# Kernel tuning notes

Measured on AMD Instinct MI355X. Metric: run time of the kernel, lower is better.

## Reference

```python
import jax, jax.numpy as jnp
import numpy as np

B, K, D, H, R, MAXP, IMG = 8, 1024, 256, 8, 4, 1024, 224


def _ln(x, g, b, eps=1e-5):
    m = x.mean(-1, keepdims=True)
    v = ((x - m) ** 2).mean(-1, keepdims=True)
    return (x - m) / jnp.sqrt(v + eps) * g + b


def _rope2d(x, coords, cache, image_size):
    b, k, d = x.shape
    half, quarter = d // 2, d // 4
    maxp = cache.shape[0]
    cn = jnp.clip(coords.astype(jnp.float32) / image_size * (maxp - 1), 0, maxp - 1)
    y_idx = cn[..., 0].astype(jnp.int32)
    x_idx = cn[..., 1].astype(jnp.int32)
    yr = cache[y_idx]  # [B,K,quarter,2]
    xr = cache[x_idx]
    xp = x[..., :half].reshape(b, k, quarter, 2)
    yp = x[..., half:].reshape(b, k, quarter, 2)

    def rot(p, r):
        c, s = r[..., 0], r[..., 1]
        p0, p1 = p[..., 0], p[..., 1]
        return jnp.stack([p0 * c - p1 * s, p0 * s + p1 * c], -1).reshape(b, k, half)

    return jnp.concatenate([rot(xp, xr), rot(yp, yr)], -1)


def _mha_zero(xn, Wqkv, bqkv, Wo, bo, key_allowed, num_heads):
    # torch MultiheadAttention with an all-zero token appended to key/value
    # BEFORE projection -> extra key = b_k, extra value = b_v per head.
    b, l, d = xn.shape
    hd = d // num_heads
    Wq, Wk, Wv = jnp.split(Wqkv, 3, axis=0)
    bq, bk, bv = jnp.split(bqkv, 3)
    q = (xn @ Wq.T + bq).reshape(b, l, num_heads, hd)
    k = jnp.concatenate([xn @ Wk.T + bk, jnp.broadcast_to(bk, (b, 1, d))], 1)
    v = jnp.concatenate([xn @ Wv.T + bv, jnp.broadcast_to(bv, (b, 1, d))], 1)
    k = k.reshape(b, l + 1, num_heads, hd)
    v = v.reshape(b, l + 1, num_heads, hd)
    scores = jnp.einsum('bqhd,bkhd->bhqk', q, k) / jnp.sqrt(jnp.float32(hd))
    mask = jnp.concatenate([key_allowed, jnp.ones((b, 1), bool)], 1)  # zero slot always visible
    scores = jnp.where(mask[:, None, None, :], scores, -jnp.inf)
    attn = jax.nn.softmax(scores, axis=-1)
    out = jnp.einsum('bhqk,bkhd->bqhd', attn, v).reshape(b, l, d)
    return out @ Wo.T + bo


def setup_inputs() -> dict:
    key = jax.random.key(0)
    ks = jax.random.split(key, 20)
    x = jax.random.normal(ks[0], (B, K, D), dtype=jnp.float32)
    coords = jax.random.randint(ks[1], (B, K, 2), 0, IMG, dtype=jnp.int32)
    ctx_id_labels = jax.random.randint(ks[2], (B, K), 0, 2, dtype=jnp.int32)
    half = D // 2
    theta = 1.0 / (10000.0 ** (jnp.arange(0, half, 2, dtype=jnp.float32) / half))
    pos = jnp.arange(MAXP, dtype=jnp.float32)
    freqs = pos[:, None] * theta[None, :]
    rope_cache = jnp.stack([jnp.cos(freqs), jnp.sin(freqs)], -1)  # [MAXP, D/4, 2]
    s = 0.02
    return {
        'x': x, 'coords': coords, 'ctx_id_labels': ctx_id_labels,
        'target_embed': s * jax.random.normal(ks[3], (1, 1, D)),
        'context_embed': s * jax.random.normal(ks[4], (1, 1, D)),
        'register_tokens': s * jax.random.normal(ks[5], (1, R, D)),
        'rope_cache': rope_cache,
        'norm_g': jnp.ones((D,)), 'norm_b': jnp.zeros((D,)),
        'ctx_Wqkv': s * jax.random.normal(ks[6], (3 * D, D)),
        'ctx_bqkv': jnp.zeros((3 * D,)),
        'ctx_Wo': s * jax.random.normal(ks[7], (D, D)),
        'ctx_bo': jnp.zeros((D,)),
        'tgt_Wqkv': s * jax.random.normal(ks[8], (3 * D, D)),
        'tgt_bqkv': jnp.zeros((3 * D,)),
        'tgt_Wo': s * jax.random.normal(ks[9], (D, D)),
        'tgt_bo': jnp.zeros((D,)),
        'mlpn_g': jnp.ones((D,)), 'mlpn_b': jnp.zeros((D,)),
        'mlp_W1': s * jax.random.normal(ks[10], (4 * D, D)),
        'mlp_b1': jnp.zeros((4 * D,)),
        'mlp_W2': s * jax.random.normal(ks[11], (D, 4 * D)),
        'mlp_b2': jnp.zeros((D,)),
    }


def reference(x, coords, ctx_id_labels, target_embed, context_embed, register_tokens,
              rope_cache, norm_g, norm_b, ctx_Wqkv, ctx_bqkv, ctx_Wo, ctx_bo,
              tgt_Wqkv, tgt_bqkv, tgt_Wo, tgt_bo, mlpn_g, mlpn_b,
              mlp_W1, mlp_b1, mlp_W2, mlp_b2):
    b, k, d = x.shape
    is_ctx = ctx_id_labels > 0
    x = x + jnp.where(is_ctx[..., None], context_embed, target_embed)
    x = _rope2d(x, coords, rope_cache, IMG)
    registers = register_tokens + context_embed  # [1,R,D]
    x = jnp.concatenate([jnp.broadcast_to(registers, (b, R, d)), x], 1)
    is_ctx_f = jnp.concatenate([jnp.ones((b, R), bool), is_ctx], 1)
    xn = _ln(x, norm_g, norm_b)
    # ctx queries self-attend to context(+zero); tgt queries cross-attend to context(+zero)
    out_ctx = _mha_zero(xn, ctx_Wqkv, ctx_bqkv, ctx_Wo, ctx_bo, is_ctx_f, H)
    out_tgt = _mha_zero(xn, tgt_Wqkv, tgt_bqkv, tgt_Wo, tgt_bo, is_ctx_f, H)
    attn_out = jnp.where(is_ctx_f[..., None], out_ctx, out_tgt)
    attn_out = attn_out[:, R:]
    x = x[:, R:]
    x = x + attn_out
    h = _ln(x, mlpn_g, mlpn_b)
    h = jax.nn.gelu(h @ mlp_W1.T + mlp_b1, approximate=False) @ mlp_W2.T + mlp_b2
    return x + h
```

## Files before the change

kernel.cpp:

```cpp
#include <hip/hip_runtime.h>
#include <stdint.h>
#include <stddef.h>

typedef unsigned short u16;
typedef __bf16 bf16t;
typedef bf16t bf16x8 __attribute__((ext_vector_type(8)));
typedef u16 u16x8 __attribute__((ext_vector_type(8)));
typedef u16 u16x4 __attribute__((ext_vector_type(4)));
typedef float f32x4 __attribute__((ext_vector_type(4)));

__device__ __forceinline__ float bf2f(u16 u) {
  unsigned int x = ((unsigned int)u) << 16;
  return __builtin_bit_cast(float, x);
}
__device__ __forceinline__ u16 f2bf(float f) {
  unsigned int x = __builtin_bit_cast(unsigned int, f);
  x += 0x7fffu + ((x >> 16) & 1u);
  return (u16)(x >> 16);
}
__device__ __forceinline__ u16x8 ld8(const u16* p) { return *(const u16x8*)p; }

__device__ __forceinline__ f32x4 mfma_bf16(u16x8 a, u16x8 b, f32x4 c) {
  return __builtin_amdgcn_mfma_f32_16x16x32_bf16(
      __builtin_bit_cast(bf16x8, a), __builtin_bit_cast(bf16x8, b), c, 0, 0, 0);
}
__device__ __forceinline__ void g2lds16(const u16* g, u16* l) {
  __builtin_amdgcn_global_load_lds(
      (const __attribute__((address_space(1))) unsigned int*)g,
      (__attribute__((address_space(3))) unsigned int*)l, 16, 0, 0);
}
__device__ __forceinline__ void stc(u16* p, float v) { *p = f2bf(v); }
__device__ __forceinline__ void stc(float* p, float v) { *p = v; }

__device__ __forceinline__ float fast_erf(float x) {
  const float ax = fabsf(x);
  const float t = 1.0f / (1.0f + 0.3275911f * ax);
  const float y = 1.0f - (((((1.061405429f * t - 1.453152027f) * t) + 1.421413741f) * t
                  - 0.284496736f) * t + 0.254829592f) * t * __expf(-ax * ax);
  return copysignf(y, x);
}


__global__ __launch_bounds__(256) void cvt_kernel(
    const float* __restrict__ cW, const float* __restrict__ tW,
    const float* __restrict__ cWo_, const float* __restrict__ tWo_,
    const float* __restrict__ W1_, const float* __restrict__ W2_,
    const float* __restrict__ cb, const float* __restrict__ tb,
    u16* __restrict__ wA, u16* __restrict__ wB, u16* __restrict__ woc,
    u16* __restrict__ wot, u16* __restrict__ w1b, u16* __restrict__ w2b,
    float* __restrict__ bA, float* __restrict__ bB,
    const int* __restrict__ labels, int* __restrict__ slotm,
    int* __restrict__ inv_c, int* __restrict__ inv_t,
    int* __restrict__ qcnt_c, int* __restrict__ qcnt_t,
    u16* __restrict__ xnc, u16* __restrict__ xnt)
{
  const int blk = blockIdx.x;
  const int tid = threadIdx.x;
  if (blk >= 1026) {
    const int b = blk - 1026;
    const int wave = tid >> 6, lane = tid & 63;
    __shared__ int wcnt[4];
    int base_c = 0, base_t = 0;
    for (int p = 0; p < 4; ++p) {
      const int idx = p * 256 + tid;
      const bool ic = labels[b * 1024 + idx] > 0;
      const unsigned long long mk = __ballot(ic);
      const int lower = __popcll(mk & ((1ull << lane) - 1ull));
      if (lane == 0) wcnt[wave] = __popcll(mk);
      __syncthreads();
      int off = 0, tot = 0;
      #pragma unroll
      for (int i = 0; i < 4; ++i) { if (i < wave) off += wcnt[i]; tot += wcnt[i]; }
      if (ic) {
        const int rank = base_c + off + lower;
        slotm[b * 1024 + idx] = rank;
        inv_c[b * 1024 + rank] = idx;
      } else {
        const int rank = base_t + tid - off - lower;
        slotm[b * 1024 + idx] = rank;
        inv_t[b * 1024 + rank] = idx;
      }
      base_c += tot; base_t += 256 - tot;
      __syncthreads();
    }
    if (tid == 0) { qcnt_c[b] = base_c; qcnt_t[b] = base_t; }
    const int nc4 = base_c + 4;
    const int needA = (nc4 + 127) & ~127;
    const int needB = (base_t + 127) & ~127;
    const u16x8 z8 = {0, 0, 0, 0, 0, 0, 0, 0};
    for (int idx = tid; idx < (needA - nc4) * 32; idx += 256)
      *(u16x8*)&xnc[((size_t)b * 1152 + nc4 + (idx >> 5)) * 256 + (idx & 31) * 8] = z8;
    for (int idx = tid; idx < (needB - base_t) * 32; idx += 256)
      *(u16x8*)&xnt[((size_t)b * 1024 + base_t + (idx >> 5)) * 256 + (idx & 31) * 8] = z8;
    return;
  }
  if (blk >= 1024) {
    const int e = tid * 4;
    if (blk == 1024) {
      #pragma unroll
      for (int j = 0; j < 4; ++j) {
        const int k = e + j;
        bA[k] = (k < 768) ? cb[k] : tb[k - 512];
      }
    } else {
      #pragma unroll
      for (int j = 0; j < 4; ++j) {
        const int k = e + j;
        if (k < 256) bA[1024 + k] = tb[512 + k];
        else if (k < 512) bB[k - 256] = tb[k - 256];
      }
    }
    return;
  }
  const float* s; u16* d;
  if (blk < 192)      { const size_t e = (size_t)blk * 1024; s = cW + e; d = wA + e; }
  else if (blk < 384) { const int lb = blk - 192; const size_t e = (size_t)lb * 1024;
                        s = tW + e; d = (lb < 64) ? (wB + e) : (wA + e + 131072); }
  else if (blk < 448) { const size_t e = (size_t)(blk - 384) * 1024; s = cWo_ + e; d = woc + e; }
  else if (blk < 512) { const size_t e = (size_t)(blk - 448) * 1024; s = tWo_ + e; d = wot + e; }
  else if (blk < 768) { const size_t e = (size_t)(blk - 512) * 1024; s = W1_ + e; d = w1b + e; }
  else                { const size_t e = (size_t)(blk - 768) * 1024; s = W2_ + e; d = w2b + e; }
  const int o = tid * 4;
  const f32x4 v = *(const f32x4*)(s + o);
  u16x4 ov;
  #pragma unroll
  for (int j = 0; j < 4; ++j) ov[j] = f2bf(v[j]);
  *(u16x4*)(d + o) = ov;
}

__global__ __launch_bounds__(256) void prep_kernel(
    const float* __restrict__ x, const int* __restrict__ coords,
    const int* __restrict__ labels, const float* __restrict__ tgt_e,
    const float* __restrict__ ctx_e, const float* __restrict__ regs,
    const float* __restrict__ rope, const float* __restrict__ g,
    const float* __restrict__ bt, const int* __restrict__ slotm,
    float* __restrict__ x0, u16* __restrict__ xnc, u16* __restrict__ xnt)
{
  const int wv = threadIdx.x >> 6, lane = threadIdx.x & 63;
  const int t = blockIdx.x * 4 + wv;
  const int d = lane * 4;
  const int b = t / 1028, l = t - b * 1028;
  f32x4 v;
  u16* dst;
  if (l < 4) {
    const f32x4 rg = *(const f32x4*)&regs[l * 256 + d];
    const f32x4 ce = *(const f32x4*)&ctx_e[d];
    #pragma unroll
    for (int j = 0; j < 4; ++j) v[j] = rg[j] + ce[j];
    dst = &xnc[((size_t)b * 1152 + l) * 256];
  } else {
    const int p = l - 4;
    const bool ic = labels[b * 1024 + p] > 0;
    const float* emb = ic ? ctx_e : tgt_e;
    const int cy = coords[(b * 1024 + p) * 2 + 0];
    const int cx = coords[(b * 1024 + p) * 2 + 1];
    const float fy = fminf(fmaxf(((float)cy / 224.0f) * 1023.0f, 0.0f), 1023.0f);
    const float fx = fminf(fmaxf(((float)cx / 224.0f) * 1023.0f, 0.0f), 1023.0f);
    const int yi = (int)fy, xi = (int)fx;
    const bool second = d >= 128;
    const int ci = second ? yi : xi;
    const int pairi = (d & 127) >> 1;
    const f32x4 rr = *(const f32x4*)&rope[ci * 128 + pairi * 2];
    const int i0 = (second ? 128 : 0) + pairi * 2;
    const size_t base = (size_t)(b * 1024 + p) * 256;
    const f32x4 xv = *(const f32x4*)&x[base + i0];
    const f32x4 ev = *(const f32x4*)&emb[i0];
    const float p0 = xv[0] + ev[0], p1 = xv[1] + ev[1];
    const float p2 = xv[2] + ev[2], p3 = xv[3] + ev[3];
    v[0] = p0 * rr[0] - p1 * rr[1];
    v[1] = p0 * rr[1] + p1 * rr[0];
    v[2] = p2 * rr[2] - p3 * rr[3];
    v[3] = p2 * rr[3] + p3 * rr[2];
    const int rank = slotm[b * 1024 + p];
    dst = ic ? &xnc[((size_t)b * 1152 + 4 + rank) * 256]
             : &xnt[((size_t)b * 1024 + rank) * 256];
  }
  *(f32x4*)&x0[(size_t)t * 256 + d] = v;
  float s1 = v[0] + v[1] + v[2] + v[3];
  #pragma unroll
  for (int off = 1; off < 64; off <<= 1) s1 += __shfl_xor(s1, off);
  const float mean = s1 * (1.0f / 256.0f);
  f32x4 dv;
  float s2 = 0.f;
  #pragma unroll
  for (int j = 0; j < 4; ++j) { dv[j] = v[j] - mean; s2 += dv[j] * dv[j]; }
  #pragma unroll
  for (int off = 1; off < 64; off <<= 1) s2 += __shfl_xor(s2, off);
  const float rstd = rsqrtf(s2 * (1.0f / 256.0f) + 1e-5f);
  const f32x4 gv = *(const f32x4*)&g[d];
  const f32x4 bv = *(const f32x4*)&bt[d];
  u16x4 o;
  #pragma unroll
  for (int j = 0; j < 4; ++j) o[j] = f2bf(dv[j] * rstd * gv[j] + bv[j]);
  *(u16x4*)&dst[d] = o;
}

template <int MI, int EPI, typename CT>
__global__ __launch_bounds__(256) void gemm_bt(
    const u16* __restrict__ A, int lda, const u16* __restrict__ W, int K,
    const float* __restrict__ bias, CT* __restrict__ C, int ldc, int M,
    const float* __restrict__ resid)
{
  constexpr int TM = MI * 32;
  const int mbase = blockIdx.y * TM, nbase = blockIdx.x * 128;
  __shared__ u16 As[TM * 32];
  __shared__ u16 Bs[128 * 32];
  const int tid = threadIdx.x, lane = tid & 63, w = tid >> 6;
  const int quad = lane >> 4, r = lane & 15;
  const int wm = w >> 1, wn = w & 1;
  const int rA = lane >> 2, cA = (lane & 3) * 8;

  f32x4 acc[MI][4];
  #pragma unroll
  for (int i = 0; i < MI; ++i)
    #pragma unroll
    for (int j = 0; j < 4; ++j) acc[i][j] = (f32x4){0.f, 0.f, 0.f, 0.f};

  const int nkt = K >> 5;
  for (int kt = 0; kt < nkt; ++kt) {
    const int k0 = kt * 32;
    #pragma unroll
    for (int j = 0; j < MI / 2; ++j) {
      const int rr = w * (MI * 8) + j * 16;
      g2lds16(&A[(size_t)(mbase + rr + rA) * lda + k0 + cA], &As[rr * 32]);
    }
    #pragma unroll
    for (int j = 0; j < 2; ++j) {
      const int rr = w * 32 + j * 16;
      g2lds16(&W[(size_t)(nbase + rr + rA) * K + k0 + cA], &Bs[rr * 32]);
    }
    __syncthreads();
    u16x8 av[MI], bv[4];
    #pragma unroll
    for (int mi = 0; mi < MI; ++mi) av[mi] = ld8(&As[(wm * (MI * 16) + mi * 16 + r) * 32 + quad * 8]);
    #pragma unroll
    for (int ni = 0; ni < 4; ++ni) bv[ni] = ld8(&Bs[(wn * 64 + ni * 16 + r) * 32 + quad * 8]);
    #pragma unroll
    for (int mi = 0; mi < MI; ++mi)
      #pragma unroll
      for (int ni = 0; ni < 4; ++ni)
        acc[mi][ni] = mfma_bf16(av[mi], bv[ni], acc[mi][ni]);
    __syncthreads();
  }

  #pragma unroll
  for (int mi = 0; mi < MI; ++mi) {
    #pragma unroll
    for (int ni = 0; ni < 4; ++ni) {
      const int col = nbase + wn * 64 + ni * 16 + r;
      const float bs = bias[col];
      const int row0 = mbase + wm * (MI * 16) + mi * 16 + quad * 4;
      #pragma unroll
      for (int i = 0; i < 4; ++i) {
        const int rr2 = row0 + i;
        if (rr2 < M) {
          float v = acc[mi][ni][i] + bs;
          if (EPI == 1) v = 0.5f * v * (1.0f + fast_erf(v * 0.70710678118654752f));
          if (EPI == 2) v += resid[(size_t)rr2 * ldc + col];
          stc(&C[(size_t)rr2 * ldc + col], v);
        }
      }
    }
  }
}

__global__ __launch_bounds__(256) void gemm_qkv(
    const u16* __restrict__ xnc, const u16* __restrict__ xnt,
    const u16* __restrict__ wA, const u16* __restrict__ wB,
    const float* __restrict__ bA, const float* __restrict__ bB,
    u16* __restrict__ qc, u16* __restrict__ qt,
    u16* __restrict__ kbuf, u16* __restrict__ vbufT,
    const int* __restrict__ qcnt_c, const int* __restrict__ qcnt_t)
{
  const int y = blockIdx.y;
  const int nbase = blockIdx.x * 128;
  const u16 *Ap, *Wp; const float* bp;
  int mbase, b;
  bool tgt;
  if (y < 72) {
    tgt = false;
    b = y / 9; const int mt = y - b * 9;
    const int need = (qcnt_c[b] + 4 + 127) & ~127;
    if (mt * 128 >= need) return;
    mbase = b * 1152 + mt * 128;
    Ap = xnc; Wp = wA; bp = bA;
  } else {
    if (nbase >= 256) return;
    tgt = true;
    const int yy = y - 72;
    b = yy >> 3; const int mt = yy & 7;
    const int need = (qcnt_t[b] + 127) & ~127;
    if (mt * 128 >= need) return;
    mbase = b * 1024 + mt * 128;
    Ap = xnt; Wp = wB; bp = bB;
  }

  __shared__ u16 As[128 * 32];
  __shared__ u16 Bs[128 * 32];
  const int tid = threadIdx.x, lane = tid & 63, w = tid >> 6;
  const int quad = lane >> 4, r = lane & 15;
  const int wm = w >> 1, wn = w & 1;
  const int rA = lane >> 2, cA = (lane & 3) * 8;

  f32x4 acc[4][4];
  #pragma unroll
  for (int i = 0; i < 4; ++i)
    #pragma unroll
    for (int j = 0; j < 4; ++j) acc[i][j] = (f32x4){0.f, 0.f, 0.f, 0.f};

  for (int kt = 0; kt < 8; ++kt) {
    const int k0 = kt * 32;
    #pragma unroll
    for (int j = 0; j < 2; ++j) {
      const int rr = w * 32 + j * 16;
      g2lds16(&Ap[(size_t)(mbase + rr + rA) * 256 + k0 + cA], &As[rr * 32]);
      g2lds16(&Wp[(size_t)(nbase + rr + rA) * 256 + k0 + cA], &Bs[rr * 32]);
    }
    __syncthreads();
    u16x8 av[4], bv[4];
    #pragma unroll
    for (int mi = 0; mi < 4; ++mi) av[mi] = ld8(&As[(wm * 64 + mi * 16 + r) * 32 + quad * 8]);
    #pragma unroll
    for (int ni = 0; ni < 4; ++ni) bv[ni] = ld8(&Bs[(wn * 64 + ni * 16 + r) * 32 + quad * 8]);
    #pragma unroll
    for (int mi = 0; mi < 4; ++mi)
      #pragma unroll
      for (int ni = 0; ni < 4; ++ni)
        acc[mi][ni] = mfma_bf16(av[mi], bv[ni], acc[mi][ni]);
    __syncthreads();
  }

  #pragma unroll
  for (int mi = 0; mi < 4; ++mi) {
    #pragma unroll
    for (int ni = 0; ni < 4; ++ni) {
      const int col = nbase + wn * 64 + ni * 16 + r;
      const float bs = bp[col];
      const int row0 = mbase + wm * 64 + mi * 16 + quad * 4;
      if (tgt) {
        #pragma unroll
        for (int i = 0; i < 4; ++i)
          qt[(size_t)(row0 + i) * 256 + col] = f2bf(acc[mi][ni][i] + bs);
      } else if (col < 256) {
        #pragma unroll
        for (int i = 0; i < 4; ++i)
          qc[(size_t)(row0 + i) * 256 + col] = f2bf(acc[mi][ni][i] + bs);
      } else {
        const int slot0 = row0 - b * 1152;
        const int u = col - 256;
        const int z = u >> 9, kv = (u >> 8) & 1, h = (u >> 5) & 7, d = u & 31;
        const size_t zbh = (size_t)(z * 8 + b) * 8 + h;
        if (kv == 0) {
          u16* kp = kbuf + zbh * 36864 + (size_t)slot0 * 32 + d;
          #pragma unroll
          for (int i = 0; i < 4; ++i) kp[i * 32] = f2bf(acc[mi][ni][i] + bs);
        } else {
          u16x4 o;
          #pragma unroll
          for (int i = 0; i < 4; ++i) o[i] = f2bf(acc[mi][ni][i] + bs);
          *(u16x4*)(vbufT + (zbh * 32 + d) * 1152 + slot0) = o;
        }
      }
    }
  }
}

__global__ __launch_bounds__(256) void gemm_wo_fused(
    const u16* __restrict__ Ac, const u16* __restrict__ At,
    const u16* __restrict__ Wc, const u16* __restrict__ Wt,
    const float* __restrict__ bc, const float* __restrict__ btg,
    const int* __restrict__ cnt_c, const int* __restrict__ cnt_t,
    const int* __restrict__ inv_c, const int* __restrict__ inv_t,
    const float* __restrict__ x0, const float* __restrict__ g,
    const float* __restrict__ bt, float* __restrict__ x1,
    u16* __restrict__ hln)
{
  const int z = blockIdx.z;
  const int y = blockIdx.y, b = y >> 4, mt = y & 15;
  const int qn = (z ? cnt_t : cnt_c)[b];
  if (mt * 64 >= ((qn + 63) & ~63)) return;
  const int mbase = b * 1024 + mt * 64;
  const u16* A = z ? At : Ac;
  const u16* W = z ? Wt : Wc;
  const float* bias = z ? btg : bc;
  const int* inv = z ? inv_t : inv_c;

  __shared__ u16 As[64 * 32];
  __shared__ u16 Bs[256 * 32];
  __shared__ float sums[2][64];
  __shared__ float sqs[2][64];
  const int tid = threadIdx.x, lane = tid & 63, w = tid >> 6;
  const int quad = lane >> 4, r = lane & 15;
  const int wm = w >> 1, wn = w & 1;
  const int rA = lane >> 2, cA = (lane & 3) * 8;

  f32x4 acc[2][8];
  #pragma unroll
  for (int i = 0; i < 2; ++i)
    #pragma unroll
    for (int j = 0; j < 8; ++j) acc[i][j] = (f32x4){0.f, 0.f, 0.f, 0.f};

  for (int kt = 0; kt < 8; ++kt) {
    const int k0 = kt * 32;
    g2lds16(&A[(size_t)(mbase + w * 16 + rA) * 256 + k0 + cA], &As[w * 512]);
    #pragma unroll
    for (int j = 0; j < 4; ++j) {
      const int rr = w * 64 + j * 16;
      g2lds16(&W[(size_t)(rr + rA) * 256 + k0 + cA], &Bs[rr * 32]);
    }
    __syncthreads();
    u16x8 av[2], bv[8];
    #pragma unroll
    for (int mi = 0; mi < 2; ++mi) av[mi] = ld8(&As[(wm * 32 + mi * 16 + r) * 32 + quad * 8]);
    #pragma unroll
    for (int ni = 0; ni < 8; ++ni) bv[ni] = ld8(&Bs[(wn * 128 + ni * 16 + r) * 32 + quad * 8]);
    #pragma unroll
    for (int mi = 0; mi < 2; ++mi)
      #pragma unroll
      for (int ni = 0; ni < 8; ++ni)
        acc[mi][ni] = mfma_bf16(av[mi], bv[ni], acc[mi][ni]);
    __syncthreads();
  }

  float biasv[8];
  #pragma unroll
  for (int ni = 0; ni < 8; ++ni) biasv[ni] = bias[wn * 128 + ni * 16 + r];

  #pragma unroll
  for (int mi = 0; mi < 2; ++mi) {
    #pragma unroll
    for (int i = 0; i < 4; ++i) {
      const int lrow = wm * 32 + mi * 16 + quad * 4 + i;
      const int slot = mt * 64 + lrow;
      const int tok = (slot < qn) ? inv[b * 1024 + slot] : 0;
      const float* x0r = &x0[((size_t)b * 1028 + 4 + tok) * 256];
      float s = 0.f, sq = 0.f;
      #pragma unroll
      for (int ni = 0; ni < 8; ++ni) {
        const float v = acc[mi][ni][i] + biasv[ni] + x0r[wn * 128 + ni * 16 + r];
        acc[mi][ni][i] = v;
        s += v; sq += v * v;
      }
      #pragma unroll
      for (int off = 1; off < 16; off <<= 1) {
        s += __shfl_xor(s, off);
        sq += __shfl_xor(sq, off);
      }
      if (r == 0) { sums[wn][lrow] = s; sqs[wn][lrow] = sq; }
    }
  }
  __syncthreads();
  #pragma unroll
  for (int mi = 0; mi < 2; ++mi) {
    #pragma unroll
    for (int i = 0; i < 4; ++i) {
      const int lrow = wm * 32 + mi * 16 + quad * 4 + i;
      const int slot = mt * 64 + lrow;
      if (slot >= qn) continue;
      const float mean = (sums[0][lrow] + sums[1][lrow]) * (1.0f / 256.0f);
      const float var = (sqs[0][lrow] + sqs[1][lrow]) * (1.0f / 256.0f) - mean * mean;
      const float rstd = rsqrtf(var + 1e-5f);
      const int tok = inv[b * 1024 + slot];
      const size_t orow = (size_t)b * 1024 + tok;
      #pragma unroll
      for (int ni = 0; ni < 8; ++ni) {
        const int col = wn * 128 + ni * 16 + r;
        const float v = acc[mi][ni][i];
        x1[orow * 256 + col] = v;
        hln[orow * 256 + col] = f2bf((v - mean) * rstd * g[col] + bt[col]);
      }
    }
  }
}

__global__ __launch_bounds__(256) void attn4_kernel(
    const u16* __restrict__ qc, const u16* __restrict__ qt,
    const u16* __restrict__ kbuf, const u16* __restrict__ vbufT,
    const float* __restrict__ cbq, const float* __restrict__ tbq,
    const int* __restrict__ qcnt_c, const int* __restrict__ qcnt_t,
    u16* __restrict__ o_c, u16* __restrict__ o_t)
{
  const int qbx = blockIdx.x, h = blockIdx.y, b = blockIdx.z;
  const int nc = qcnt_c[b], nt = qcnt_t[b];
  const int cblk = (nc + 63) >> 6, tblk = (nt + 63) >> 6;
  int z, qsb, qn;
  if (qbx < cblk)            { z = 0; qsb = qbx << 6; qn = nc; }
  else if (qbx - cblk < tblk){ z = 1; qsb = (qbx - cblk) << 6; qn = nt; }
  else return;
  const int nc4 = nc + 4;
  const int ntile = (nc4 + 63) >> 6;
  const float* bq = z ? tbq : cbq;
  const u16* Q = z ? qt : qc;
  u16* obuf = z ? o_t : o_c;
  const int qrow0 = z ? (b * 1024 + qsb) : (b * 1152 + 4 + qsb);

  const int tid = threadIdx.x, lane = tid & 63, w = tid >> 6;
  const int quad = lane >> 4, r = lane & 15;
  const float scale = 0.17677669529663687f;

  __shared__ u16 Ks[2][2048];
  __shared__ u16 Vt[2][32 * 66];
  __shared__ u16 Ps[4][16 * 72];

  const u16x8 qf = ld8(&Q[(size_t)(qrow0 + w * 16 + r) * 256 + h * 32 + quad * 8]);

  float s0 = 0.f;
  #pragma unroll
  for (int j = 0; j < 8; ++j) s0 += bf2f(qf[j]) * bq[256 + h * 32 + quad * 8 + j];
  s0 *= scale;
  s0 += __shfl_xor(s0, 16);
  s0 += __shfl_xor(s0, 32);
  float m_ = s0, l_ = 1.0f;
  f32x4 accA, accB;
  #pragma unroll
  for (int i = 0; i < 4; ++i) {
    accA[i] = bq[512 + h * 32 + quad * 4 + i];
    accB[i] = bq[512 + h * 32 + 16 + quad * 4 + i];
  }

  const size_t zbh = (size_t)(z * 8 + b) * 8 + h;
  const u16* kz = kbuf + zbh * 36864;
  const u16* vz = vbufT + zbh * 36864;
  const int dloc = (w << 3) + (lane >> 3), part = lane & 7;

  g2lds16(&kz[w * 512 + lane * 8], &Ks[0][w * 512]);
  u16x8 vv = ld8(&vz[(size_t)dloc * 1152 + part * 8]);

  for (int t = 0; t < ntile; ++t) {
    const int cur = t & 1, nxt = cur ^ 1;
    #pragma unroll
    for (int j = 0; j < 8; ++j) Vt[cur][dloc * 66 + part * 8 + j] = vv[j];
    __syncthreads();
    if (t + 1 < ntile) {
      g2lds16(&kz[(t + 1) * 2048 + w * 512 + lane * 8], &Ks[nxt][w * 512]);
      vv = ld8(&vz[(size_t)dloc * 1152 + (t + 1) * 64 + part * 8]);
    }

    f32x4 sT[4];
    #pragma unroll
    for (int tt = 0; tt < 4; ++tt) {
      const u16x8 kf = ld8(&Ks[cur][(tt * 16 + r) * 32 + quad * 8]);
      sT[tt] = mfma_bf16(kf, qf, (f32x4){0.f, 0.f, 0.f, 0.f});
    }
    const int kb0 = t * 64 + quad * 4;
    float rm = -3.0e38f;
    float sc[4][4];
    #pragma unroll
    for (int tt = 0; tt < 4; ++tt)
      #pragma unroll
      for (int i = 0; i < 4; ++i) {
        const float kbias = (kb0 + tt * 16 + i < nc4) ? 0.0f : -1e30f;
        sc[tt][i] = sT[tt][i] * scale + kbias;
        rm = fmaxf(rm, sc[tt][i]);
      }
    rm = fmaxf(rm, __shfl_xor(rm, 16));
    rm = fmaxf(rm, __shfl_xor(rm, 32));
    const float mn = fmaxf(m_, rm);
    const float al = __expf(m_ - mn);
    m_ = mn;
    float rs = 0.f;
    u16* ps = &Ps[w][r * 72];
    #pragma unroll
    for (int tt = 0; tt < 4; ++tt) {
      u16x4 pk;
      #pragma unroll
      for (int i = 0; i < 4; ++i) {
        const float pv = __expf(sc[tt][i] - mn);
        rs += pv;
        pk[i] = f2bf(pv);
      }
      *(u16x4*)&ps[tt * 16 + quad * 4] = pk;
    }
    rs += __shfl_xor(rs, 16);
    rs += __shfl_xor(rs, 32);
    l_ = l_ * al + rs;
    #pragma unroll
    for (int i = 0; i < 4; ++i) { accA[i] *= al; accB[i] *= al; }
    #pragma unroll
    for (int kk = 0; kk < 2; ++kk) {
      const u16x8 pf = ld8(&Ps[w][r * 72 + kk * 32 + quad * 8]);
      const u16x8 vf0 = ld8(&Vt[cur][r * 66 + kk * 32 + quad * 8]);
      const u16x8 vf1 = ld8(&Vt[cur][(16 + r) * 66 + kk * 32 + quad * 8]);
      accA = mfma_bf16(vf0, pf, accA);
      accB = mfma_bf16(vf1, pf, accB);
    }
  }

  const int qlocal = qsb + w * 16 + r;
  if (qlocal < qn) {
    const float inv = 1.0f / l_;
    u16x4 oa, ob;
    #pragma unroll
    for (int i = 0; i < 4; ++i) { oa[i] = f2bf(accA[i] * inv); ob[i] = f2bf(accB[i] * inv); }
    const size_t orow = (size_t)b * 1024 + qlocal;
    *(u16x4*)&obuf[orow * 256 + h * 32 + quad * 4] = oa;
    *(u16x4*)&obuf[orow * 256 + h * 32 + 16 + quad * 4] = ob;
  }
}

extern "C" void kernel_launch(void* const* d_in, const int* in_sizes, int n_in,
                              void* d_out, int out_size, void* d_ws, size_t ws_size,
                              hipStream_t stream) {
  const float* x      = (const float*)d_in[0];
  const int*   coords = (const int*)d_in[1];
  const int*   labels = (const int*)d_in[2];
  const float* tgt_e  = (const float*)d_in[3];
  const float* ctx_e  = (const float*)d_in[4];
  const float* regs   = (const float*)d_in[5];
  const float* rope   = (const float*)d_in[6];
  const float* ng     = (const float*)d_in[7];
  const float* nb     = (const float*)d_in[8];
  const float* cWqkv  = (const float*)d_in[9];
  const float* cbqkv  = (const float*)d_in[10];
  const float* cWo    = (const float*)d_in[11];
  const float* cbo    = (const float*)d_in[12];
  const float* tWqkv  = (const float*)d_in[13];
  const float* tbqkv  = (const float*)d_in[14];
  const float* tWo    = (const float*)d_in[15];
  const float* tbo    = (const float*)d_in[16];
  const float* mg     = (const float*)d_in[17];
  const float* mbeta  = (const float*)d_in[18];
  const float* W1     = (const float*)d_in[19];
  const float* b1     = (const float*)d_in[20];
  const float* W2     = (const float*)d_in[21];
  const float* b2     = (const float*)d_in[22];

  char* ws = (char*)d_ws;
  float* x0     = (float*)(ws + 0);
  u16*   qc     = (u16*)  (ws + 8421376);
  u16*   xnc    = (u16*)  (ws + 13139968);
  u16*   xnt    = (u16*)  (ws + 17858560);
  u16*   qt     = (u16*)  (ws + 22052864);
  u16*   kbuf   = (u16*)  (ws + 26247168);
  u16*   vbufT  = (u16*)  (ws + 35684352);
  u16*   o_c    = (u16*)  (ws + 45121536);
  u16*   o_t    = (u16*)  (ws + 49315840);
  u16*   wA     = (u16*)  (ws + 53510144);
  u16*   wB     = (u16*)  (ws + 54165504);
  u16*   woc    = (u16*)  (ws + 54296576);
  u16*   wot    = (u16*)  (ws + 54427648);
  u16*   w1b    = (u16*)  (ws + 54558720);
  u16*   w2b    = (u16*)  (ws + 55083008);
  float* bA     = (float*)(ws + 55607296);
  float* bB     = (float*)(ws + 55612416);
  int*   slotm  = (int*)  (ws + 55613440);
  int*   inv_c  = (int*)  (ws + 55646208);
  int*   inv_t  = (int*)  (ws + 55678976);
  int*   qcnt_c = (int*)  (ws + 55711744);
  int*   qcnt_t = (int*)  (ws + 55711776);
  u16*   hln    = (u16*)  (ws + 17858560);
  float* x1     = (float*)(ws + 26247168);
  u16*   hmid   = (u16*)  (ws + 35684352);

  cvt_kernel<<<dim3(1034), 256, 0, stream>>>(cWqkv, tWqkv, cWo, tWo, W1, W2,
                                             cbqkv, tbqkv,
                                             wA, wB, woc, wot, w1b, w2b, bA, bB,
                                             labels, slotm, inv_c, inv_t,
                                             qcnt_c, qcnt_t, xnc, xnt);
  prep_kernel<<<dim3(2056), 256, 0, stream>>>(x, coords, labels, tgt_e, ctx_e,
                                              regs, rope, ng, nb, slotm, x0, xnc, xnt);
  gemm_qkv<<<dim3(10, 136), 256, 0, stream>>>(xnc, xnt, wA, wB, bA, bB,
                                              qc, qt, kbuf, vbufT, qcnt_c, qcnt_t);
  attn4_kernel<<<dim3(17, 8, 8), 256, 0, stream>>>(qc, qt, kbuf, vbufT, cbqkv, tbqkv,
                                                   qcnt_c, qcnt_t, o_c, o_t);
  gemm_wo_fused<<<dim3(1, 128, 2), 256, 0, stream>>>(o_c, o_t, woc, wot, cbo, tbo,
                                                     qcnt_c, qcnt_t, inv_c, inv_t,
                                                     x0, mg, mbeta, x1, hln);
  gemm_bt<4, 1, u16><<<dim3(8, 64), 256, 0, stream>>>(hln, 256, w1b, 256, b1, hmid, 1024, 8192, nullptr);
  gemm_bt<2, 2, float><<<dim3(2, 128), 256, 0, stream>>>(hmid, 1024, w2b, 1024, b2, (float*)d_out, 256, 8192, x1);
}
```

Baseline: 228.4 us.

## Process two query strips per attention block, shrink Wo tiles, move weight casts into prep

The attention kernel now handles two 64-query strips per block, so each K/V tile loaded into LDS is reused by both strips and the grid shrinks from 17 to 9 blocks in x. The Wo+LayerNorm GEMM drops from 64-row to 32-row tiles, doubling its block count to spread work across more CUs. The weight bf16 conversion moves from the compaction kernel into extra blocks of the prep kernel, leaving a small 10-block compaction kernel. Costs include higher register pressure in attention, less tail parallelism there, and more redundant weight loads per row in the Wo GEMM.

New measurement: 220.8 us. 3.3% less time.

```diff
diff --git a/kernel.cpp b/kernel.cpp
--- a/kernel.cpp
+++ b/kernel.cpp
@@ -41,62 +41,19 @@
 }
 
 
-__global__ __launch_bounds__(256) void cvt_kernel(
-    const float* __restrict__ cW, const float* __restrict__ tW,
-    const float* __restrict__ cWo_, const float* __restrict__ tWo_,
-    const float* __restrict__ W1_, const float* __restrict__ W2_,
-    const float* __restrict__ cb, const float* __restrict__ tb,
-    u16* __restrict__ wA, u16* __restrict__ wB, u16* __restrict__ woc,
-    u16* __restrict__ wot, u16* __restrict__ w1b, u16* __restrict__ w2b,
-    float* __restrict__ bA, float* __restrict__ bB,
+__global__ __launch_bounds__(256) void compact_kernel(
     const int* __restrict__ labels, int* __restrict__ slotm,
     int* __restrict__ inv_c, int* __restrict__ inv_t,
     int* __restrict__ qcnt_c, int* __restrict__ qcnt_t,
-    u16* __restrict__ xnc, u16* __restrict__ xnt)
+    u16* __restrict__ xnc, u16* __restrict__ xnt,
+    const float* __restrict__ cb, const float* __restrict__ tb,
+    float* __restrict__ bA, float* __restrict__ bB)
 {
   const int blk = blockIdx.x;
   const int tid = threadIdx.x;
-  if (blk >= 1026) {
-    const int b = blk - 1026;
-    const int wave = tid >> 6, lane = tid & 63;
-    __shared__ int wcnt[4];
-    int base_c = 0, base_t = 0;
-    for (int p = 0; p < 4; ++p) {
-      const int idx = p * 256 + tid;
-      const bool ic = labels[b * 1024 + idx] > 0;
-      const unsigned long long mk = __ballot(ic);
-      const int lower = __popcll(mk & ((1ull << lane) - 1ull));
-      if (lane == 0) wcnt[wave] = __popcll(mk);
-      __syncthreads();
-      int off = 0, tot = 0;
-      #pragma unroll
-      for (int i = 0; i < 4; ++i) { if (i < wave) off += wcnt[i]; tot += wcnt[i]; }
-      if (ic) {
-        const int rank = base_c + off + lower;
-        slotm[b * 1024 + idx] = rank;
-        inv_c[b * 1024 + rank] = idx;
-      } else {
-        const int rank = base_t + tid - off - lower;
-        slotm[b * 1024 + idx] = rank;
-        inv_t[b * 1024 + rank] = idx;
-      }
-      base_c += tot; base_t += 256 - tot;
-      __syncthreads();
-    }
-    if (tid == 0) { qcnt_c[b] = base_c; qcnt_t[b] = base_t; }
-    const int nc4 = base_c + 4;
-    const int needA = (nc4 + 127) & ~127;
-    const int needB = (base_t + 127) & ~127;
-    const u16x8 z8 = {0, 0, 0, 0, 0, 0, 0, 0};
-    for (int idx = tid; idx < (needA - nc4) * 32; idx += 256)
-      *(u16x8*)&xnc[((size_t)b * 1152 + nc4 + (idx >> 5)) * 256 + (idx & 31) * 8] = z8;
-    for (int idx = tid; idx < (needB - base_t) * 32; idx += 256)
-      *(u16x8*)&xnt[((size_t)b * 1024 + base_t + (idx >> 5)) * 256 + (idx & 31) * 8] = z8;
-    return;
-  }
-  if (blk >= 1024) {
+  if (blk >= 8) {
     const int e = tid * 4;
-    if (blk == 1024) {
+    if (blk == 8) {
       #pragma unroll
       for (int j = 0; j < 4; ++j) {
         const int k = e + j;
@@ -112,20 +69,41 @@
     }
     return;
   }
-  const float* s; u16* d;
-  if (blk < 192)      { const size_t e = (size_t)blk * 1024; s = cW + e; d = wA + e; }
-  else if (blk < 384) { const int lb = blk - 192; const size_t e = (size_t)lb * 1024;
-                        s = tW + e; d = (lb < 64) ? (wB + e) : (wA + e + 131072); }
-  else if (blk < 448) { const size_t e = (size_t)(blk - 384) * 1024; s = cWo_ + e; d = woc + e; }
-  else if (blk < 512) { const size_t e = (size_t)(blk - 448) * 1024; s = tWo_ + e; d = wot + e; }
-  else if (blk < 768) { const size_t e = (size_t)(blk - 512) * 1024; s = W1_ + e; d = w1b + e; }
-  else                { const size_t e = (size_t)(blk - 768) * 1024; s = W2_ + e; d = w2b + e; }
-  const int o = tid * 4;
-  const f32x4 v = *(const f32x4*)(s + o);
-  u16x4 ov;
-  #pragma unroll
-  for (int j = 0; j < 4; ++j) ov[j] = f2bf(v[j]);
-  *(u16x4*)(d + o) = ov;
+  const int b = blk;
+  const int wave = tid >> 6, lane = tid & 63;
+  __shared__ int wcnt[4];
+  int base_c = 0, base_t = 0;
+  for (int p = 0; p < 4; ++p) {
+    const int idx = p * 256 + tid;
+    const bool ic = labels[b * 1024 + idx] > 0;
+    const unsigned long long mk = __ballot(ic);
+    const int lower = __popcll(mk & ((1ull << lane) - 1ull));
+    if (lane == 0) wcnt[wave] = __popcll(mk);
+    __syncthreads();
+    int off = 0, tot = 0;
+    #pragma unroll
+    for (int i = 0; i < 4; ++i) { if (i < wave) off += wcnt[i]; tot += wcnt[i]; }
+    if (ic) {
+      const int rank = base_c + off + lower;
+      slotm[b * 1024 + idx] = rank;
+      inv_c[b * 1024 + rank] = idx;
+    } else {
+      const int rank = base_t + tid - off - lower;
+      slotm[b * 1024 + idx] = rank;
+      inv_t[b * 1024 + rank] = idx;
+    }
+    base_c += tot; base_t += 256 - tot;
+    __syncthreads();
+  }
+  if (tid == 0) { qcnt_c[b] = base_c; qcnt_t[b] = base_t; }
+  const int nc4 = base_c + 4;
+  const int needA = (nc4 + 127) & ~127;
+  const int needB = (base_t + 127) & ~127;
+  const u16x8 z8 = {0, 0, 0, 0, 0, 0, 0, 0};
+  for (int idx = tid; idx < (needA - nc4) * 32; idx += 256)
+    *(u16x8*)&xnc[((size_t)b * 1152 + nc4 + (idx >> 5)) * 256 + (idx & 31) * 8] = z8;
+  for (int idx = tid; idx < (needB - base_t) * 32; idx += 256)
+    *(u16x8*)&xnt[((size_t)b * 1024 + base_t + (idx >> 5)) * 256 + (idx & 31) * 8] = z8;
 }
 
 __global__ __launch_bounds__(256) void prep_kernel(
@@ -134,8 +112,31 @@
     const float* __restrict__ ctx_e, const float* __restrict__ regs,
     const float* __restrict__ rope, const float* __restrict__ g,
     const float* __restrict__ bt, const int* __restrict__ slotm,
-    float* __restrict__ x0, u16* __restrict__ xnc, u16* __restrict__ xnt)
+    float* __restrict__ x0, u16* __restrict__ xnc, u16* __restrict__ xnt,
+    const float* __restrict__ cW, const float* __restrict__ tW,
+    const float* __restrict__ cWo_, const float* __restrict__ tWo_,
+    const float* __restrict__ W1_, const float* __restrict__ W2_,
+    u16* __restrict__ wA, u16* __restrict__ wB, u16* __restrict__ woc,
+    u16* __restrict__ wot, u16* __restrict__ w1b, u16* __restrict__ w2b)
 {
+  if (blockIdx.x >= 2056) {
+    const int blk = blockIdx.x - 2056;
+    const float* s; u16* d;
+    if (blk < 192)      { const size_t e = (size_t)blk * 1024; s = cW + e; d = wA + e; }
+    else if (blk < 384) { const int lb = blk - 192; const size_t e = (size_t)lb * 1024;
+                          s = tW + e; d = (lb < 64) ? (wB + e) : (wA + e + 131072); }
+    else if (blk < 448) { const size_t e = (size_t)(blk - 384) * 1024; s = cWo_ + e; d = woc + e; }
+    else if (blk < 512) { const size_t e = (size_t)(blk - 448) * 1024; s = tWo_ + e; d = wot + e; }
+    else if (blk < 768) { const size_t e = (size_t)(blk - 512) * 1024; s = W1_ + e; d = w1b + e; }
+    else                { const size_t e = (size_t)(blk - 768) * 1024; s = W2_ + e; d = w2b + e; }
+    const int o = threadIdx.x * 4;
+    const f32x4 v = *(const f32x4*)(s + o);
+    u16x4 ov;
+    #pragma unroll
+    for (int j = 0; j < 4; ++j) ov[j] = f2bf(v[j]);
+    *(u16x4*)(d + o) = ov;
+    return;
+  }
   const int wv = threadIdx.x >> 6, lane = threadIdx.x & 63;
   const int t = blockIdx.x * 4 + wv;
   const int d = lane * 4;
@@ -376,49 +377,43 @@
     u16* __restrict__ hln)
 {
   const int z = blockIdx.z;
-  const int y = blockIdx.y, b = y >> 4, mt = y & 15;
+  const int y = blockIdx.y, b = y >> 5, mt = y & 31;
   const int qn = (z ? cnt_t : cnt_c)[b];
-  if (mt * 64 >= ((qn + 63) & ~63)) return;
-  const int mbase = b * 1024 + mt * 64;
+  if (mt * 32 >= ((qn + 31) & ~31)) return;
+  const int mbase = b * 1024 + mt * 32;
   const u16* A = z ? At : Ac;
   const u16* W = z ? Wt : Wc;
   const float* bias = z ? btg : bc;
   const int* inv = z ? inv_t : inv_c;
 
-  __shared__ u16 As[64 * 32];
+  __shared__ u16 As[32 * 32];
   __shared__ u16 Bs[256 * 32];
-  __shared__ float sums[2][64];
-  __shared__ float sqs[2][64];
+  __shared__ float sums[2][32];
+  __shared__ float sqs[2][32];
   const int tid = threadIdx.x, lane = tid & 63, w = tid >> 6;
   const int quad = lane >> 4, r = lane & 15;
   const int wm = w >> 1, wn = w & 1;
   const int rA = lane >> 2, cA = (lane & 3) * 8;
 
-  f32x4 acc[2][8];
-  #pragma unroll
-  for (int i = 0; i < 2; ++i)
-    #pragma unroll
-    for (int j = 0; j < 8; ++j) acc[i][j] = (f32x4){0.f, 0.f, 0.f, 0.f};
+  f32x4 acc[8];
+  #pragma unroll
+  for (int j = 0; j < 8; ++j) acc[j] = (f32x4){0.f, 0.f, 0.f, 0.f};
 
   for (int kt = 0; kt < 8; ++kt) {
     const int k0 = kt * 32;
-    g2lds16(&A[(size_t)(mbase + w * 16 + rA) * 256 + k0 + cA], &As[w * 512]);
+    if (w < 2) g2lds16(&A[(size_t)(mbase + w * 16 + rA) * 256 + k0 + cA], &As[w * 512]);
     #pragma unroll
     for (int j = 0; j < 4; ++j) {
       const int rr = w * 64 + j * 16;
       g2lds16(&W[(size_t)(rr + rA) * 256 + k0 + cA], &Bs[rr * 32]);
     }
     __syncthreads();
-    u16x8 av[2], bv[8];
-    #pragma unroll
-    for (int mi = 0; mi < 2; ++mi) av[mi] = ld8(&As[(wm * 32 + mi * 16 + r) * 32 + quad * 8]);
+    const u16x8 av = ld8(&As[(wm * 16 + r) * 32 + quad * 8]);
+    u16x8 bv[8];
     #pragma unroll
     for (int ni = 0; ni < 8; ++ni) bv[ni] = ld8(&Bs[(wn * 128 + ni * 16 + r) * 32 + quad * 8]);
     #pragma unroll
-    for (int mi = 0; mi < 2; ++mi)
-      #pragma unroll
-      for (int ni = 0; ni < 8; ++ni)
-        acc[mi][ni] = mfma_bf16(av[mi], bv[ni], acc[mi][ni]);
+    for (int ni = 0; ni < 8; ++ni) acc[ni] = mfma_bf16(av, bv[ni], acc[ni]);
     __syncthreads();
   }
 
@@ -427,72 +422,70 @@
   for (int ni = 0; ni < 8; ++ni) biasv[ni] = bias[wn * 128 + ni * 16 + r];
 
   #pragma unroll
-  for (int mi = 0; mi < 2; ++mi) {
-    #pragma unroll
-    for (int i = 0; i < 4; ++i) {
-      const int lrow = wm * 32 + mi * 16 + quad * 4 + i;
-      const int slot = mt * 64 + lrow;
-      const int tok = (slot < qn) ? inv[b * 1024 + slot] : 0;
-      const float* x0r = &x0[((size_t)b * 1028 + 4 + tok) * 256];
-      float s = 0.f, sq = 0.f;
-      #pragma unroll
-      for (int ni = 0; ni < 8; ++ni) {
-        const float v = acc[mi][ni][i] + biasv[ni] + x0r[wn * 128 + ni * 16 + r];
-        acc[mi][ni][i] = v;
-        s += v; sq += v * v;
-      }
-      #pragma unroll
-      for (int off = 1; off < 16; off <<= 1) {
-        s += __shfl_xor(s, off);
-        sq += __shfl_xor(sq, off);
-      }
-      if (r == 0) { sums[wn][lrow] = s; sqs[wn][lrow] = sq; }
-    }
+  for (int i = 0; i < 4; ++i) {
+    const int lrow = wm * 16 + quad * 4 + i;
+    const int slot = mt * 32 + lrow;
+    const int tok = (slot < qn) ? inv[b * 1024 + slot] : 0;
+    const float* x0r = &x0[((size_t)b * 1028 + 4 + tok) * 256];
+    float s = 0.f, sq = 0.f;
+    #pragma unroll
+    for (int ni = 0; ni < 8; ++ni) {
+      const float v = acc[ni][i] + biasv[ni] + x0r[wn * 128 + ni * 16 + r];
+      acc[ni][i] = v;
+      s += v; sq += v * v;
+    }
+    #pragma unroll
+    for (int off = 1; off < 16; off <<= 1) {
+      s += __shfl_xor(s, off);
+      sq += __shfl_xor(sq, off);
+    }
+    if (r == 0) { sums[wn][lrow] = s; sqs[wn][lrow] = sq; }
   }
   __syncthreads();
   #pragma unroll
-  for (int mi = 0; mi < 2; ++mi) {
-    #pragma unroll
-    for (int i = 0; i < 4; ++i) {
-      const int lrow = wm * 32 + mi * 16 + quad * 4 + i;
-      const int slot = mt * 64 + lrow;
-      if (slot >= qn) continue;
-      const float mean = (sums[0][lrow] + sums[1][lrow]) * (1.0f / 256.0f);
-      const float var = (sqs[0][lrow] + sqs[1][lrow]) * (1.0f / 256.0f) - mean * mean;
-      const float rstd = rsqrtf(var + 1e-5f);
-      const int tok = inv[b * 1024 + slot];
-      const size_t orow = (size_t)b * 1024 + tok;
-      #pragma unroll
-      for (int ni = 0; ni < 8; ++ni) {
-        const int col = wn * 128 + ni * 16 + r;
-        const float v = acc[mi][ni][i];
-        x1[orow * 256 + col] = v;
-        hln[orow * 256 + col] = f2bf((v - mean) * rstd * g[col] + bt[col]);
-      }
-    }
-  }
-}
-
-__global__ __launch_bounds__(256) void attn4_kernel(
+  for (int i = 0; i < 4; ++i) {
+    const int lrow = wm * 16 + quad * 4 + i;
+    const int slot = mt * 32 + lrow;
+    if (slot >= qn) continue;
+    const float mean = (sums[0][lrow] + sums[1][lrow]) * (1.0f / 256.0f);
+    const float var = (sqs[0][lrow] + sqs[1][lrow]) * (1.0f / 256.0f) - mean * mean;
+    const float rstd = rsqrtf(var + 1e-5f);
+    const int tok = inv[b * 1024 + slot];
+    const size_t orow = (size_t)b * 1024 + tok;
+    #pragma unroll
+    for (int ni = 0; ni < 8; ++ni) {
+      const int col = wn * 128 + ni * 16 + r;
+      const float v = acc[ni][i];
+      x1[orow * 256 + col] = v;
+      hln[orow * 256 + col] = f2bf((v - mean) * rstd * g[col] + bt[col]);
+    }
+  }
+}
+
+__global__ __launch_bounds__(256) void attn5_kernel(
     const u16* __restrict__ qc, const u16* __restrict__ qt,
     const u16* __restrict__ kbuf, const u16* __restrict__ vbufT,
     const float* __restrict__ cbq, const float* __restrict__ tbq,
     const int* __restrict__ qcnt_c, const int* __restrict__ qcnt_t,
     u16* __restrict__ o_c, u16* __restrict__ o_t)
 {
-  const int qbx = blockIdx.x, h = blockIdx.y, b = blockIdx.z;
+  const int px = blockIdx.x, h = blockIdx.y, b = blockIdx.z;
   const int nc = qcnt_c[b], nt = qcnt_t[b];
   const int cblk = (nc + 63) >> 6, tblk = (nt + 63) >> 6;
-  int z, qsb, qn;
-  if (qbx < cblk)            { z = 0; qsb = qbx << 6; qn = nc; }
-  else if (qbx - cblk < tblk){ z = 1; qsb = (qbx - cblk) << 6; qn = nt; }
+  const int cpair = (cblk + 1) >> 1, tpair = (tblk + 1) >> 1;
+  int z, sblk, qn, nblk;
+  if (px < cpair)            { z = 0; sblk = px * 2; qn = nc; nblk = cblk; }
+  else if (px - cpair < tpair){ z = 1; sblk = (px - cpair) * 2; qn = nt; nblk = tblk; }
   else return;
+  const int nstrip = (nblk - sblk >= 2) ? 2 : 1;
   const int nc4 = nc + 4;
   const int ntile = (nc4 + 63) >> 6;
   const float* bq = z ? tbq : cbq;
   const u16* Q = z ? qt : qc;
   u16* obuf = z ? o_t : o_c;
-  const int qrow0 = z ? (b * 1024 + qsb) : (b * 1152 + 4 + qsb);
+  const int qrowbase = z ? (b * 1024) : (b * 1152 + 4);
+  const int qsb0 = sblk * 64;
+  const int qsb1 = (nstrip > 1) ? qsb0 + 64 : qsb0;
 
   const int tid = threadIdx.x, lane = tid & 63, w = tid >> 6;
   const int quad = lane >> 4, r = lane & 15;
@@ -502,20 +495,27 @@
   __shared__ u16 Vt[2][32 * 66];
   __shared__ u16 Ps[4][16 * 72];
 
-  const u16x8 qf = ld8(&Q[(size_t)(qrow0 + w * 16 + r) * 256 + h * 32 + quad * 8]);
-
-  float s0 = 0.f;
-  #pragma unroll
-  for (int j = 0; j < 8; ++j) s0 += bf2f(qf[j]) * bq[256 + h * 32 + quad * 8 + j];
-  s0 *= scale;
-  s0 += __shfl_xor(s0, 16);
-  s0 += __shfl_xor(s0, 32);
-  float m_ = s0, l_ = 1.0f;
-  f32x4 accA, accB;
+  const u16x8 qf0 = ld8(&Q[(size_t)(qrowbase + qsb0 + w * 16 + r) * 256 + h * 32 + quad * 8]);
+  const u16x8 qf1 = ld8(&Q[(size_t)(qrowbase + qsb1 + w * 16 + r) * 256 + h * 32 + quad * 8]);
+
+  float s0a = 0.f, s0b = 0.f;
+  #pragma unroll
+  for (int j = 0; j < 8; ++j) {
+    const float bk = bq[256 + h * 32 + quad * 8 + j];
+    s0a += bf2f(qf0[j]) * bk;
+    s0b += bf2f(qf1[j]) * bk;
+  }
+  s0a *= scale; s0b *= scale;
+  s0a += __shfl_xor(s0a, 16); s0a += __shfl_xor(s0a, 32);
+  s0b += __shfl_xor(s0b, 16); s0b += __shfl_xor(s0b, 32);
+  float m0 = s0a, l0 = 1.0f, m1 = s0b, l1 = 1.0f;
+  f32x4 accA0, accB0, accA1, accB1;
   #pragma unroll
   for (int i = 0; i < 4; ++i) {
-    accA[i] = bq[512 + h * 32 + quad * 4 + i];
-    accB[i] = bq[512 + h * 32 + 16 + quad * 4 + i];
+    accA0[i] = bq[512 + h * 32 + quad * 4 + i];
+    accB0[i] = bq[512 + h * 32 + 16 + quad * 4 + i];
+    accA1[i] = accA0[i];
+    accB1[i] = accB0[i];
   }
 
   const size_t zbh = (size_t)(z * 8 + b) * 8 + h;
@@ -535,66 +535,84 @@
       g2lds16(&kz[(t + 1) * 2048 + w * 512 + lane * 8], &Ks[nxt][w * 512]);
       vv = ld8(&vz[(size_t)dloc * 1152 + (t + 1) * 64 + part * 8]);
     }
-
-    f32x4 sT[4];
-    #pragma unroll
-    for (int tt = 0; tt < 4; ++tt) {
-      const u16x8 kf = ld8(&Ks[cur][(tt * 16 + r) * 32 + quad * 8]);
-      sT[tt] = mfma_bf16(kf, qf, (f32x4){0.f, 0.f, 0.f, 0.f});
-    }
     const int kb0 = t * 64 + quad * 4;
-    float rm = -3.0e38f;
-    float sc[4][4];
-    #pragma unroll
-    for (int tt = 0; tt < 4; ++tt)
-      #pragma unroll
-      for (int i = 0; i < 4; ++i) {
-        const float kbias = (kb0 + tt * 16 + i < nc4) ? 0.0f : -1e30f;
-        sc[tt][i] = sT[tt][i] * scale + kbias;
-        rm = fmaxf(rm, sc[tt][i]);
+
+    auto strip = [&](const u16x8& qf, float& m_, float& l_, f32x4& accA, f32x4& accB) {
+      f32x4 sT[4];
+      #pragma unroll
+      for (int tt = 0; tt < 4; ++tt) {
+        const u16x8 kf = ld8(&Ks[cur][(tt * 16 + r) * 32 + quad * 8]);
+        sT[tt] = mfma_bf16(kf, qf, (f32x4){0.f, 0.f, 0.f, 0.f});
       }
-    rm = fmaxf(rm, __shfl_xor(rm, 16));
-    rm = fmaxf(rm, __shfl_xor(rm, 32));
-    const float mn = fmaxf(m_, rm);
-    const float al = __expf(m_ - mn);
-    m_ = mn;
-    float rs = 0.f;
-    u16* ps = &Ps[w][r * 72];
-    #pragma unroll
-    for (int tt = 0; tt < 4; ++tt) {
-      u16x4 pk;
-      #pragma unroll
-      for (int i = 0; i < 4; ++i) {
-        const float pv = __expf(sc[tt][i] - mn);
-        rs += pv;
-        pk[i] = f2bf(pv);
+      float rm = -3.0e38f;
+      float sc[4][4];
+      #pragma unroll
+      for (int tt = 0; tt < 4; ++tt)
+        #pragma unroll
+        for (int i = 0; i < 4; ++i) {
+          const float kbias = (kb0 + tt * 16 + i < nc4) ? 0.0f : -1e30f;
+          sc[tt][i] = sT[tt][i] * scale + kbias;
+          rm = fmaxf(rm, sc[tt][i]);
+        }
+      rm = fmaxf(rm, __shfl_xor(rm, 16));
+      rm = fmaxf(rm, __shfl_xor(rm, 32));
+      const float mn = fmaxf(m_, rm);
+      const float al = __expf(m_ - mn);
+      m_ = mn;
+      float rs = 0.f;
+      u16* ps = &Ps[w][r * 72];
+      #pragma unroll
+      for (int tt = 0; tt < 4; ++tt) {
+        u16x4 pk;
+        #pragma unroll
+        for (int i = 0; i < 4; ++i) {
+          const float pv = __expf(sc[tt][i] - mn);
+          rs += pv;
+          pk[i] = f2bf(pv);
+        }
+        *(u16x4*)&ps[tt * 16 + quad * 4] = pk;
       }
-      *(u16x4*)&ps[tt * 16 + quad * 4] = pk;
-    }
-    rs += __shfl_xor(rs, 16);
-    rs += __shfl_xor(rs, 32);
-    l_ = l_ * al + rs;
-    #pragma unroll
-    for (int i = 0; i < 4; ++i) { accA[i] *= al; accB[i] *= al; }
-    #pragma unroll
-    for (int kk = 0; kk < 2; ++kk) {
-      const u16x8 pf = ld8(&Ps[w][r * 72 + kk * 32 + quad * 8]);
-      const u16x8 vf0 = ld8(&Vt[cur][r * 66 + kk * 32 + quad * 8]);
-      const u16x8 vf1 = ld8(&Vt[cur][(16 + r) * 66 + kk * 32 + quad * 8]);
-      accA = mfma_bf16(vf0, pf, accA);
-      accB = mfma_bf16(vf1, pf, accB);
-    }
-  }
-
-  const int qlocal = qsb + w * 16 + r;
-  if (qlocal < qn) {
-    const float inv = 1.0f / l_;
-    u16x4 oa, ob;
-    #pragma unroll
-    for (int i = 0; i < 4; ++i) { oa[i] = f2bf(accA[i] * inv); ob[i] = f2bf(accB[i] * inv); }
-    const size_t orow = (size_t)b * 1024 + qlocal;
-    *(u16x4*)&obuf[orow * 256 + h * 32 + quad * 4] = oa;
-    *(u16x4*)&obuf[orow * 256 + h * 32 + 16 + quad * 4] = ob;
+      rs += __shfl_xor(rs, 16);
+      rs += __shfl_xor(rs, 32);
+      l_ = l_ * al + rs;
+      #pragma unroll
+      for (int i = 0; i < 4; ++i) { accA[i] *= al; accB[i] *= al; }
+      #pragma unroll
+      for (int kk = 0; kk < 2; ++kk) {
+        const u16x8 pf = ld8(&Ps[w][r * 72 + kk * 32 + quad * 8]);
+        const u16x8 vf0 = ld8(&Vt[cur][r * 66 + kk * 32 + quad * 8]);
+        const u16x8 vf1 = ld8(&Vt[cur][(16 + r) * 66 + kk * 32 + quad * 8]);
+        accA = mfma_bf16(vf0, pf, accA);
+        accB = mfma_bf16(vf1, pf, accB);
+      }
+    };
+    strip(qf0, m0, l0, accA0, accB0);
+    if (nstrip > 1) strip(qf1, m1, l1, accA1, accB1);
+  }
+
+  {
+    const int qlocal = qsb0 + w * 16 + r;
+    if (qlocal < qn) {
+      const float inv = 1.0f / l0;
+      u16x4 oa, ob;
+      #pragma unroll
+      for (int i = 0; i < 4; ++i) { oa[i] = f2bf(accA0[i] * inv); ob[i] = f2bf(accB0[i] * inv); }
+      const size_t orow = (size_t)b * 1024 + qlocal;
+      *(u16x4*)&obuf[orow * 256 + h * 32 + quad * 4] = oa;
+      *(u16x4*)&obuf[orow * 256 + h * 32 + 16 + quad * 4] = ob;
+    }
+  }
+  if (nstrip > 1) {
+    const int qlocal = qsb1 + w * 16 + r;
+    if (qlocal < qn) {
+      const float inv = 1.0f / l1;
+      u16x4 oa, ob;
+      #pragma unroll
+      for (int i = 0; i < 4; ++i) { oa[i] = f2bf(accA1[i] * inv); ob[i] = f2bf(accB1[i] * inv); }
+      const size_t orow = (size_t)b * 1024 + qlocal;
+      *(u16x4*)&obuf[orow * 256 + h * 32 + quad * 4] = oa;
+      *(u16x4*)&obuf[orow * 256 + h * 32 + 16 + quad * 4] = ob;
+    }
   }
 }
 
@@ -652,18 +670,18 @@
   float* x1     = (float*)(ws + 26247168);
   u16*   hmid   = (u16*)  (ws + 35684352);
 
-  cvt_kernel<<<dim3(1034), 256, 0, stream>>>(cWqkv, tWqkv, cWo, tWo, W1, W2,
-                                             cbqkv, tbqkv,
-                                             wA, wB, woc, wot, w1b, w2b, bA, bB,
-                                             labels, slotm, inv_c, inv_t,
-                                             qcnt_c, qcnt_t, xnc, xnt);
-  prep_kernel<<<dim3(2056), 256, 0, stream>>>(x, coords, labels, tgt_e, ctx_e,
-                                              regs, rope, ng, nb, slotm, x0, xnc, xnt);
+  compact_kernel<<<dim3(10), 256, 0, stream>>>(labels, slotm, inv_c, inv_t,
+                                               qcnt_c, qcnt_t, xnc, xnt,
+                                               cbqkv, tbqkv, bA, bB);
+  prep_kernel<<<dim3(3080), 256, 0, stream>>>(x, coords, labels, tgt_e, ctx_e,
+                                              regs, rope, ng, nb, slotm, x0, xnc, xnt,
+                                              cWqkv, tWqkv, cWo, tWo, W1, W2,
+                                              wA, wB, woc, wot, w1b, w2b);
   gemm_qkv<<<dim3(10, 136), 256, 0, stream>>>(xnc, xnt, wA, wB, bA, bB,
                                               qc, qt, kbuf, vbufT, qcnt_c, qcnt_t);
-  attn4_kernel<<<dim3(17, 8, 8), 256, 0, stream>>>(qc, qt, kbuf, vbufT, cbqkv, tbqkv,
-                                                   qcnt_c, qcnt_t, o_c, o_t);
-  gemm_wo_fused<<<dim3(1, 128, 2), 256, 0, stream>>>(o_c, o_t, woc, wot, cbo, tbo,
+  attn5_kernel<<<dim3(9, 8, 8), 256, 0, stream>>>(qc, qt, kbuf, vbufT, cbqkv, tbqkv,
+                                                  qcnt_c, qcnt_t, o_c, o_t);
+  gemm_wo_fused<<<dim3(1, 256, 2), 256, 0, stream>>>(o_c, o_t, woc, wot, cbo, tbo,
                                                      qcnt_c, qcnt_t, inv_c, inv_t,
                                                      x0, mg, mbeta, x1, hln);
   gemm_bt<4, 1, u16><<<dim3(8, 64), 256, 0, stream>>>(hln, 256, w1b, 256, b1, hmid, 1024, 8192, nullptr);
```
